# Kernel optimization log

Hardware: AMD Instinct MI355X
Metric: run time of the kernel (lower is better)

The kernel has to match this reference:

```python
import jax, jax.numpy as jnp
import numpy as np

LN_EPS = 1e-5

def _layernorm(x, g, b):
    mu = jnp.mean(x, axis=-1, keepdims=True)
    var = jnp.var(x, axis=-1, keepdims=True)
    return (x - mu) * jax.lax.rsqrt(var + LN_EPS) * g + b

def setup_inputs() -> dict:
    key = jax.random.key(0)
    ks = jax.random.split(key, 8)
    B, T, V, H = 32, 128, 204, 128
    s = 0.02
    x = jax.random.normal(ks[0], (B, T, V, 1), dtype=jnp.float32)
    return {
        "x": x,
        # batched per-variable GRN params
        "fc1_w": jax.random.normal(ks[1], (V, H), dtype=jnp.float32) * s,
        "fc1_b": jnp.zeros((V, H), jnp.float32),
        "fc2_w": jax.random.normal(ks[2], (V, H, H), dtype=jnp.float32) * s,
        "fc2_b": jnp.zeros((V, H), jnp.float32),
        "glu_w": jax.random.normal(ks[3], (V, 2 * H, H), dtype=jnp.float32) * s,
        "glu_b": jnp.zeros((V, 2 * H), jnp.float32),
        "skip_w": jax.random.normal(ks[4], (V, H), dtype=jnp.float32) * s,
        "skip_b": jnp.zeros((V, H), jnp.float32),
        "ln_g": jnp.ones((H,), jnp.float32),
        "ln_b": jnp.zeros((H,), jnp.float32),
        # weight GRN params (input_dim=V, hidden=H, output_dim=V; identity skip)
        "wfc1_w": jax.random.normal(ks[5], (V, H), dtype=jnp.float32) * s,
        "wfc1_b": jnp.zeros((H,), jnp.float32),
        "wfc2_w": jax.random.normal(ks[6], (H, H), dtype=jnp.float32) * s,
        "wfc2_b": jnp.zeros((H,), jnp.float32),
        "wglu_w": jax.random.normal(ks[7], (H, 2 * V), dtype=jnp.float32) * s,
        "wglu_b": jnp.zeros((2 * V,), jnp.float32),
        "wln_g": jnp.ones((V,), jnp.float32),
        "wln_b": jnp.zeros((V,), jnp.float32),
    }

def reference(x, fc1_w, fc1_b, fc2_w, fc2_b, glu_w, glu_b, skip_w, skip_b, ln_g, ln_b,
              wfc1_w, wfc1_b, wfc2_w, wfc2_b, wglu_w, wglu_b, wln_g, wln_b):
    B, T, V, D = x.shape
    H = fc1_w.shape[1]
    xs = x.reshape(B * T, V)  # (N, V) since D == 1

    # --- batched per-variable GRN (eval mode: dropout is identity) ---
    h = jax.nn.elu(xs[..., None] * fc1_w + fc1_b)              # (N, V, H)
    h = jnp.einsum('nvh,vhk->nvk', h, fc2_w) + fc2_b           # bmm over V
    glu = jnp.einsum('nvh,vgh->nvg', h, glu_w) + glu_b         # (N, V, 2H)
    fc_out, gate = glu[..., :H], glu[..., H:]
    h = fc_out * jax.nn.sigmoid(gate)
    skip = xs[..., None] * skip_w + skip_b                     # (N, V, H)
    var_out = _layernorm(skip + h, ln_g, ln_b)                 # (N, V, H)

    # --- weight GRN (input_dim = output_dim = V -> identity skip) ---
    a = jax.nn.elu(xs @ wfc1_w + wfc1_b)                       # (N, H)
    a = a @ wfc2_w + wfc2_b
    g = a @ wglu_w + wglu_b                                    # (N, 2V)
    hg = g[:, :V] * jax.nn.sigmoid(g[:, V:])
    wts = jax.nn.softmax(_layernorm(xs + hg, wln_g, wln_b), axis=-1)  # (N, V)

    out = jnp.einsum('nvh,nv->nh', var_out, wts)               # (N, H)
    return out.reshape(B, T, H), wts.reshape(B, T, V)
```

## Files before the change

### kernel.cpp

```cpp
#include <hip/hip_runtime.h>
#include <hip/hip_bf16.h>

#define NROWS 4096
#define NV    204
#define NH    128
#define NG    256

#define SLOT_B     16384
#define SMS_OFF    (3 * SLOT_B)
#define SMS_BYTES  3584
#define LN_OFF     (SMS_OFF + 2 * SMS_BYTES)
#define LDS_BYTES  (LN_OFF + 1024)

typedef __bf16 bf16x8 __attribute__((ext_vector_type(8)));
typedef float  f32x4  __attribute__((ext_vector_type(4)));

__device__ __forceinline__ float elu_f(float x)  { return x > 0.f ? x : __expf(x) - 1.f; }
__device__ __forceinline__ float sigm_f(float x) { return 1.f / (1.f + __expf(-x)); }

__device__ __forceinline__ void stage16(const void* g, void* l) {
    __builtin_amdgcn_global_load_lds((const __attribute__((address_space(1))) void*)g,
                                     (__attribute__((address_space(3))) void*)l, 16, 0, 0);
}

__device__ __forceinline__ void stage_half(const void* src, char* dst, int w, int l) {
    const char* sb = (const char*)src;
    #pragma unroll
    for (int s = 0; s < 4; ++s)
        stage16(sb + (w * 4 + s) * 1024 + l * 16, dst + (w * 4 + s) * 1024);
}

__device__ __forceinline__ void stage_smalls(const float* src, char* dst, int w, int l) {
    if (w < 3)       stage16((const char*)src + w * 1024 + l * 16, dst + w * 1024);
    else if (l < 32) stage16((const char*)src + 3072 + l * 16,     dst + 3072);
}

#define PSYNC(N) do { \
    asm volatile("s_waitcnt vmcnt(" N ")" ::: "memory"); \
    __builtin_amdgcn_s_barrier(); \
    asm volatile("" ::: "memory"); \
} while (0)

#define NB_FC2 NV
#define NB_GLU (NV * 16)
#define NB_SM  NV
#define NB_WTS (NROWS / 8)

__global__ __launch_bounds__(256) void k_setup(
    const float* __restrict__ fc2_w, __bf16* __restrict__ fc2t,
    const float* __restrict__ glu_w, __bf16* __restrict__ glu16,
    const float* __restrict__ fc1_w, const float* __restrict__ fc1_b,
    const float* __restrict__ fc2_b, const float* __restrict__ glu_b,
    const float* __restrict__ skip_w, const float* __restrict__ skip_b,
    float* __restrict__ smalls,
    const float* __restrict__ xs,
    const float* __restrict__ wfc1_w, const float* __restrict__ wfc1_b,
    const float* __restrict__ wfc2_w, const float* __restrict__ wfc2_b,
    const float* __restrict__ wglu_w, const float* __restrict__ wglu_b,
    const float* __restrict__ wln_g,  const float* __restrict__ wln_b,
    float* __restrict__ wts)
{
    __shared__ float tile[64 * 129];
    __shared__ float sx[8][NV];
    __shared__ float sa[8][NH];
    __shared__ float sg[8][2 * NV];

    const int b = blockIdx.x;
    const int t = threadIdx.x;

    if (b < NB_FC2) {
        const int v = b;
        const float* s = fc2_w + (size_t)v * (NH * NH);
        __bf16*      d = fc2t + (size_t)v * (NH * NH);
        for (int h = 0; h < 2; ++h) {
            __syncthreads();
            for (int i = t; i < 64 * 32; i += 256) {
                const int k = i >> 5, n4 = (i & 31) * 4;
                const float4 f = *(const float4*)(s + (h * 64 + k) * 128 + n4);
                tile[k * 129 + n4 + 0] = f.x;
                tile[k * 129 + n4 + 1] = f.y;
                tile[k * 129 + n4 + 2] = f.z;
                tile[k * 129 + n4 + 3] = f.w;
            }
            __syncthreads();
            for (int i = t; i < 128 * 8; i += 256) {
                const int n = i >> 3, kc = (i & 7) * 8;
                bf16x8 o;
                #pragma unroll
                for (int q = 0; q < 8; ++q) o[q] = (__bf16)tile[(kc + q) * 129 + n];
                const int ch  = h * 8 + (i & 7);
                const int chs = ch ^ (n & 15);
                *(bf16x8*)(d + n * 128 + chs * 8) = o;
            }
        }
        return;
    }

    if (b < NB_FC2 + NB_GLU) {
        const int idx = (b - NB_FC2) * 256 + t;
        const int ch = idx & 15;
        const int g  = (idx >> 4) & 255;
        const int v  = idx >> 12;
        const float* sp = glu_w + (((size_t)v * NG + g) * NH + ch * 8);
        const float4 f0 = *(const float4*)(sp);
        const float4 f1 = *(const float4*)(sp + 4);
        bf16x8 o;
        o[0] = (__bf16)f0.x; o[1] = (__bf16)f0.y; o[2] = (__bf16)f0.z; o[3] = (__bf16)f0.w;
        o[4] = (__bf16)f1.x; o[5] = (__bf16)f1.y; o[6] = (__bf16)f1.z; o[7] = (__bf16)f1.w;
        const int dch = ch ^ (g & 15);
        *(bf16x8*)(glu16 + (((size_t)v * NG + g) * NH) + dch * 8) = o;
        return;
    }

    if (b < NB_FC2 + NB_GLU + NB_SM) {
        const int v = b - (NB_FC2 + NB_GLU);
        float* dst = smalls + (size_t)v * 1024;
        for (int idx = t; idx < 896; idx += 256) {
            float val;
            if      (idx < 128)  val = fc1_w[v * NH + idx];
            else if (idx < 256)  val = fc1_b[v * NH + idx - 128];
            else if (idx < 384)  val = fc2_b[v * NH + idx - 256];
            else if (idx < 640)  val = glu_b[v * NG + idx - 384];
            else if (idx < 768)  val = skip_w[v * NH + idx - 640];
            else                 val = skip_b[v * NH + idx - 768];
            dst[idx] = val;
        }
        return;
    }

    const int r0 = (b - NB_FC2 - NB_GLU - NB_SM) * 8;
    const int tr = t >> 5;
    const int tc = t & 31;

    for (int i = t; i < 8 * NV; i += 256) {
        const int r = i / NV, c = i - r * NV;
        sx[r][c] = xs[(size_t)(r0 + r) * NV + c];
    }
    __syncthreads();

    float acc1[4];
    #pragma unroll
    for (int j = 0; j < 4; ++j) acc1[j] = wfc1_b[tc + 32 * j];
    for (int v = 0; v < NV; ++v) {
        const float xv = sx[tr][v];
        #pragma unroll
        for (int j = 0; j < 4; ++j)
            acc1[j] = fmaf(xv, wfc1_w[v * NH + tc + 32 * j], acc1[j]);
    }
    #pragma unroll
    for (int j = 0; j < 4; ++j) sa[tr][tc + 32 * j] = elu_f(acc1[j]);
    __syncthreads();

    float acc2[4];
    #pragma unroll
    for (int j = 0; j < 4; ++j) acc2[j] = wfc2_b[tc + 32 * j];
    for (int h = 0; h < NH; ++h) {
        const float av = sa[tr][h];
        #pragma unroll
        for (int j = 0; j < 4; ++j)
            acc2[j] = fmaf(av, wfc2_w[h * NH + tc + 32 * j], acc2[j]);
    }
    __syncthreads();
    #pragma unroll
    for (int j = 0; j < 4; ++j) sa[tr][tc + 32 * j] = acc2[j];
    __syncthreads();

    float accg[13];
    #pragma unroll
    for (int gi = 0; gi < 12; ++gi) accg[gi] = wglu_b[tc + 32 * gi];
    accg[12] = (tc < 24) ? wglu_b[tc + 384] : 0.f;
    for (int h = 0; h < NH; ++h) {
        const float av = sa[tr][h];
        #pragma unroll
        for (int gi = 0; gi < 12; ++gi)
            accg[gi] = fmaf(av, wglu_w[h * (2 * NV) + tc + 32 * gi], accg[gi]);
        if (tc < 24) accg[12] = fmaf(av, wglu_w[h * (2 * NV) + tc + 384], accg[12]);
    }
    __syncthreads();
    #pragma unroll
    for (int gi = 0; gi < 12; ++gi) sg[tr][tc + 32 * gi] = accg[gi];
    if (tc < 24) sg[tr][tc + 384] = accg[12];
    __syncthreads();

    float tv[7];
    float s1 = 0.f, s2 = 0.f;
    #pragma unroll
    for (int ii = 0; ii < 7; ++ii) {
        const int c = tc + 32 * ii;
        float val = 0.f;
        if (c < NV) {
            const float hg = sg[tr][c] * sigm_f(sg[tr][c + NV]);
            val = sx[tr][c] + hg;
            s1 += val; s2 = fmaf(val, val, s2);
        }
        tv[ii] = val;
    }
    #pragma unroll
    for (int m = 1; m <= 16; m <<= 1) { s1 += __shfl_xor(s1, m); s2 += __shfl_xor(s2, m); }
    const float mu  = s1 * (1.f / 204.f);
    const float var = s2 * (1.f / 204.f) - mu * mu;
    const float rs  = rsqrtf(fmaxf(var, 0.f) + 1e-5f);

    float mx = -1e30f;
    #pragma unroll
    for (int ii = 0; ii < 7; ++ii) {
        const int c = tc + 32 * ii;
        if (c < NV) {
            const float y = fmaf((tv[ii] - mu) * rs, wln_g[c], wln_b[c]);
            tv[ii] = y;
            mx = fmaxf(mx, y);
        }
    }
    #pragma unroll
    for (int m = 1; m <= 16; m <<= 1) mx = fmaxf(mx, __shfl_xor(mx, m));
    float se = 0.f;
    #pragma unroll
    for (int ii = 0; ii < 7; ++ii) {
        const int c = tc + 32 * ii;
        if (c < NV) {
            const float e = __expf(tv[ii] - mx);
            tv[ii] = e;
            se += e;
        }
    }
    #pragma unroll
    for (int m = 1; m <= 16; m <<= 1) se += __shfl_xor(se, m);
    const float inv = 1.f / se;
    #pragma unroll
    for (int ii = 0; ii < 7; ++ii) {
        const int c = tc + 32 * ii;
        if (c < NV) wts[(size_t)(r0 + tr) * NV + c] = tv[ii] * inv;
    }
}

__global__ __launch_bounds__(256, 2) void k_main(
    const float*  __restrict__ xs,
    const __bf16* __restrict__ fc2t,
    const __bf16* __restrict__ glu16,
    const float*  __restrict__ smalls,
    const float*  __restrict__ ln_g,
    const float*  __restrict__ ln_b,
    const float*  __restrict__ wts,
    float*        __restrict__ out)
{
    __shared__ __align__(16) char lds[LDS_BYTES];

    const int tid = threadIdx.x;
    const int w   = tid >> 6;
    const int l   = tid & 63;
    const int l15 = l & 15;
    const int lg  = l >> 4;

    const int vg = blockIdx.x & 7;
    const int m0 = (blockIdx.x >> 3) * 64 + w * 16;
    const int nv = (NV - 1 - vg) / 8 + 1;
    const size_t rowoff = (size_t)(m0 + l15) * NV;

    char* const slot0 = lds;
    char* const slot1 = lds + SLOT_B;
    char* const slot2 = lds + 2 * SLOT_B;

    const f32x4 zero4 = {0.f, 0.f, 0.f, 0.f};
    f32x4 acc_out[8];
    #pragma unroll
    for (int j = 0; j < 8; ++j) acc_out[j] = zero4;

    const int  sh0 = l15 + ((lg & 1) << 5);
    const int  sh1 = sh0 + 16;
    const bool rlo = (lg < 2);

    const float* lnS = (const float*)(lds + LN_OFF);

    float xv, wv, xn, wn;
    {
        if (w == 0) {
            const char* p = (l < 32) ? ((const char*)ln_g + l * 16)
                                     : ((const char*)ln_b + (l - 32) * 16);
            stage16(p, lds + LN_OFF);
        }
        stage_half(fc2t + (size_t)vg * (NH * NH), slot0, w, l);
        stage_smalls(smalls + (size_t)vg * 1024, lds + SMS_OFF, w, l);
        stage_half(fc2t + (size_t)vg * (NH * NH) + 64 * NH, slot1, w, l);
        xv = xs[rowoff + vg];
        wv = wts[rowoff + vg];
    }

    for (int i = 0; i < nv; ++i) {
        const int v  = vg + 8 * i;
        const int vn = (i + 1 < nv) ? v + 8 : v;
        const float* sm = (const float*)(lds + SMS_OFF + (i & 1) * SMS_BYTES);
        const __bf16* gluv = glu16 + (size_t)v * (NG * NH);

        PSYNC("6");
        stage_half(gluv, slot2, w, l);

        bf16x8 a1[4];
        #pragma unroll
        for (int kb = 0; kb < 4; ++kb) {
            const int k0 = kb * 32 + lg * 8;
            const float4 w0 = *(const float4*)(sm + k0);
            const float4 w1 = *(const float4*)(sm + k0 + 4);
            const float4 b0 = *(const float4*)(sm + 128 + k0);
            const float4 b1 = *(const float4*)(sm + 128 + k0 + 4);
            bf16x8 af;
            af[0] = (__bf16)elu_f(fmaf(xv, w0.x, b0.x));
            af[1] = (__bf16)elu_f(fmaf(xv, w0.y, b0.y));
            af[2] = (__bf16)elu_f(fmaf(xv, w0.z, b0.z));
            af[3] = (__bf16)elu_f(fmaf(xv, w0.w, b0.w));
            af[4] = (__bf16)elu_f(fmaf(xv, w1.x, b1.x));
            af[5] = (__bf16)elu_f(fmaf(xv, w1.y, b1.y));
            af[6] = (__bf16)elu_f(fmaf(xv, w1.z, b1.z));
            af[7] = (__bf16)elu_f(fmaf(xv, w1.w, b1.w));
            a1[kb] = af;
        }

        f32x4 h2f[8];
        __builtin_amdgcn_s_setprio(1);
        #pragma unroll
        for (int j = 0; j < 4; ++j) {
            f32x4 acc = *(const f32x4*)(sm + 256 + j * 16 + lg * 4);
            const char* rp = slot0 + (j * 16 + l15) * 256;
            #pragma unroll
            for (int kb = 0; kb < 4; ++kb) {
                const bf16x8 wf = *(const bf16x8*)(rp + (((kb * 4 + lg) ^ l15) << 4));
                acc = __builtin_amdgcn_mfma_f32_16x16x32_bf16(wf, a1[kb], acc, 0, 0, 0);
            }
            h2f[j] = acc;
        }
        __builtin_amdgcn_s_setprio(0);

        PSYNC("6");
        stage_half(gluv + 64 * NH, slot0, w, l);

        __builtin_amdgcn_s_setprio(1);
        #pragma unroll
        for (int j = 4; j < 8; ++j) {
            f32x4 acc = *(const f32x4*)(sm + 256 + j * 16 + lg * 4);
            const char* rp = slot1 + ((j - 4) * 16 + l15) * 256;
            #pragma unroll
            for (int kb = 0; kb < 4; ++kb) {
                const bf16x8 wf = *(const bf16x8*)(rp + (((kb * 4 + lg) ^ l15) << 4));
                acc = __builtin_amdgcn_mfma_f32_16x16x32_bf16(wf, a1[kb], acc, 0, 0, 0);
            }
            h2f[j] = acc;
        }
        __builtin_amdgcn_s_setprio(0);

        bf16x8 b2[4];
        #pragma unroll
        for (int kb2 = 0; kb2 < 4; ++kb2) {
            union U { __bf16 h[4]; int i2[2]; };
            U P, Q;
            P.h[0] = (__bf16)h2f[2 * kb2 + 0][0]; P.h[1] = (__bf16)h2f[2 * kb2 + 0][1];
            P.h[2] = (__bf16)h2f[2 * kb2 + 0][2]; P.h[3] = (__bf16)h2f[2 * kb2 + 0][3];
            Q.h[0] = (__bf16)h2f[2 * kb2 + 1][0]; Q.h[1] = (__bf16)h2f[2 * kb2 + 1][1];
            Q.h[2] = (__bf16)h2f[2 * kb2 + 1][2]; Q.h[3] = (__bf16)h2f[2 * kb2 + 1][3];
            const int px0 = __shfl(P.i2[0], sh0), qx0 = __shfl(Q.i2[0], sh0);
            const int py0 = __shfl(P.i2[1], sh0), qy0 = __shfl(Q.i2[1], sh0);
            const int px1 = __shfl(P.i2[0], sh1), qx1 = __shfl(Q.i2[0], sh1);
            const int py1 = __shfl(P.i2[1], sh1), qy1 = __shfl(Q.i2[1], sh1);
            union V { int ii[4]; bf16x8 vv; } R;
            R.ii[0] = rlo ? px0 : qx0;
            R.ii[1] = rlo ? py0 : qy0;
            R.ii[2] = rlo ? px1 : qx1;
            R.ii[3] = rlo ? py1 : qy1;
            b2[kb2] = R.vv;
        }

        PSYNC("4");
        stage_half(gluv + 128 * NH, slot1, w, l);

        f32x4 fco[8];
        __builtin_amdgcn_s_setprio(1);
        #pragma unroll
        for (int j = 0; j < 4; ++j) {
            f32x4 acc = *(const f32x4*)(sm + 384 + j * 16 + lg * 4);
            const char* rp = slot2 + (j * 16 + l15) * 256;
            #pragma unroll
            for (int kb = 0; kb < 4; ++kb) {
                const bf16x8 wf = *(const bf16x8*)(rp + (((kb * 4 + lg) ^ l15) << 4));
                acc = __builtin_amdgcn_mfma_f32_16x16x32_bf16(wf, b2[kb], acc, 0, 0, 0);
            }
            fco[j] = acc;
        }
        __builtin_amdgcn_s_setprio(0);

        PSYNC("4");
        stage_half(gluv + 192 * NH, slot2, w, l);

        __builtin_amdgcn_s_setprio(1);
        #pragma unroll
        for (int j = 4; j < 8; ++j) {
            f32x4 acc = *(const f32x4*)(sm + 384 + j * 16 + lg * 4);
            const char* rp = slot0 + ((j - 4) * 16 + l15) * 256;
            #pragma unroll
            for (int kb = 0; kb < 4; ++kb) {
                const bf16x8 wf = *(const bf16x8*)(rp + (((kb * 4 + lg) ^ l15) << 4));
                acc = __builtin_amdgcn_mfma_f32_16x16x32_bf16(wf, b2[kb], acc, 0, 0, 0);
            }
            fco[j] = acc;
        }
        __builtin_amdgcn_s_setprio(0);

        PSYNC("4");
        stage_half(fc2t + (size_t)vn * (NH * NH), slot0, w, l);

        f32x4 sv[8];
        __builtin_amdgcn_s_setprio(1);
        #pragma unroll
        for (int j = 0; j < 4; ++j) {
            f32x4 acc = *(const f32x4*)(sm + 512 + j * 16 + lg * 4);
            const char* rp = slot1 + (j * 16 + l15) * 256;
            #pragma unroll
            for (int kb = 0; kb < 4; ++kb) {
                const bf16x8 wg = *(const bf16x8*)(rp + (((kb * 4 + lg) ^ l15) << 4));
                acc = __builtin_amdgcn_mfma_f32_16x16x32_bf16(wg, b2[kb], acc, 0, 0, 0);
            }
            __builtin_amdgcn_s_setprio(0);
            const float4 sw4 = *(const float4*)(sm + 640 + j * 16 + lg * 4);
            const float4 sb4 = *(const float4*)(sm + 768 + j * 16 + lg * 4);
            f32x4 s;
            s[0] = fmaf(xv, sw4.x, sb4.x) + fco[j][0] * sigm_f(acc[0]);
            s[1] = fmaf(xv, sw4.y, sb4.y) + fco[j][1] * sigm_f(acc[1]);
            s[2] = fmaf(xv, sw4.z, sb4.z) + fco[j][2] * sigm_f(acc[2]);
            s[3] = fmaf(xv, sw4.w, sb4.w) + fco[j][3] * sigm_f(acc[3]);
            sv[j] = s;
            __builtin_amdgcn_s_setprio(1);
        }
        __builtin_amdgcn_s_setprio(0);

        PSYNC("4");
        stage_smalls(smalls + (size_t)vn * 1024,
                     lds + SMS_OFF + ((i + 1) & 1) * SMS_BYTES, w, l);
        stage_half(fc2t + (size_t)vn * (NH * NH) + 64 * NH, slot1, w, l);
        xn = xs[rowoff + vn];
        wn = wts[rowoff + vn];

        __builtin_amdgcn_s_setprio(1);
        #pragma unroll
        for (int j = 4; j < 8; ++j) {
            f32x4 acc = *(const f32x4*)(sm + 512 + j * 16 + lg * 4);
            const char* rp = slot2 + ((j - 4) * 16 + l15) * 256;
            #pragma unroll
            for (int kb = 0; kb < 4; ++kb) {
                const bf16x8 wg = *(const bf16x8*)(rp + (((kb * 4 + lg) ^ l15) << 4));
                acc = __builtin_amdgcn_mfma_f32_16x16x32_bf16(wg, b2[kb], acc, 0, 0, 0);
            }
            __builtin_amdgcn_s_setprio(0);
            const float4 sw4 = *(const float4*)(sm + 640 + j * 16 + lg * 4);
            const float4 sb4 = *(const float4*)(sm + 768 + j * 16 + lg * 4);
            f32x4 s;
            s[0] = fmaf(xv, sw4.x, sb4.x) + fco[j][0] * sigm_f(acc[0]);
            s[1] = fmaf(xv, sw4.y, sb4.y) + fco[j][1] * sigm_f(acc[1]);
            s[2] = fmaf(xv, sw4.z, sb4.z) + fco[j][2] * sigm_f(acc[2]);
            s[3] = fmaf(xv, sw4.w, sb4.w) + fco[j][3] * sigm_f(acc[3]);
            sv[j] = s;
            __builtin_amdgcn_s_setprio(1);
        }
        __builtin_amdgcn_s_setprio(0);

        float t1 = 0.f, t2 = 0.f;
        #pragma unroll
        for (int j = 0; j < 8; ++j) {
            #pragma unroll
            for (int r = 0; r < 4; ++r) { t1 += sv[j][r]; t2 = fmaf(sv[j][r], sv[j][r], t2); }
        }
        t1 += __shfl_xor(t1, 16); t2 += __shfl_xor(t2, 16);
        t1 += __shfl_xor(t1, 32); t2 += __shfl_xor(t2, 32);
        const float mu  = t1 * (1.f / 128.f);
        const float var = t2 * (1.f / 128.f) - mu * mu;
        const float rsv = rsqrtf(fmaxf(var, 0.f) + 1e-5f);

        #pragma unroll
        for (int j = 0; j < 8; ++j) {
            const float4 lg4 = *(const float4*)(lnS + j * 16 + lg * 4);
            const float4 lb4 = *(const float4*)(lnS + 128 + j * 16 + lg * 4);
            const float y0 = fmaf((sv[j][0] - mu) * rsv, lg4.x, lb4.x);
            const float y1 = fmaf((sv[j][1] - mu) * rsv, lg4.y, lb4.y);
            const float y2 = fmaf((sv[j][2] - mu) * rsv, lg4.z, lb4.z);
            const float y3 = fmaf((sv[j][3] - mu) * rsv, lg4.w, lb4.w);
            acc_out[j][0] = fmaf(wv, y0, acc_out[j][0]);
            acc_out[j][1] = fmaf(wv, y1, acc_out[j][1]);
            acc_out[j][2] = fmaf(wv, y2, acc_out[j][2]);
            acc_out[j][3] = fmaf(wv, y3, acc_out[j][3]);
        }

        xv = xn; wv = wn;
    }

    asm volatile("s_waitcnt vmcnt(0)" ::: "memory");

    #pragma unroll
    for (int j = 0; j < 8; ++j) {
        #pragma unroll
        for (int r = 0; r < 4; ++r)
            atomicAdd(&out[(size_t)(m0 + l15) * NH + j * 16 + lg * 4 + r], acc_out[j][r]);
    }
}

extern "C" void kernel_launch(void* const* d_in, const int* in_sizes, int n_in,
                              void* d_out, int out_size, void* d_ws, size_t ws_size,
                              hipStream_t stream) {
    (void)in_sizes; (void)n_in; (void)out_size; (void)ws_size;

    const float* xs     = (const float*)d_in[0];
    const float* fc1_w  = (const float*)d_in[1];
    const float* fc1_b  = (const float*)d_in[2];
    const float* fc2_w  = (const float*)d_in[3];
    const float* fc2_b  = (const float*)d_in[4];
    const float* glu_w  = (const float*)d_in[5];
    const float* glu_b  = (const float*)d_in[6];
    const float* skip_w = (const float*)d_in[7];
    const float* skip_b = (const float*)d_in[8];
    const float* ln_g   = (const float*)d_in[9];
    const float* ln_b   = (const float*)d_in[10];
    const float* wfc1_w = (const float*)d_in[11];
    const float* wfc1_b = (const float*)d_in[12];
    const float* wfc2_w = (const float*)d_in[13];
    const float* wfc2_b = (const float*)d_in[14];
    const float* wglu_w = (const float*)d_in[15];
    const float* wglu_b = (const float*)d_in[16];
    const float* wln_g  = (const float*)d_in[17];
    const float* wln_b  = (const float*)d_in[18];

    float* out = (float*)d_out;
    float* wts = out + (size_t)NROWS * NH;

    __bf16* fc2t   = (__bf16*)d_ws;
    __bf16* glu16  = fc2t + (size_t)NV * NH * NH;
    float*  smalls = (float*)(glu16 + (size_t)NV * NG * NH);

    hipMemsetAsync(d_out, 0, (size_t)NROWS * NH * sizeof(float), stream);

    k_setup<<<NB_FC2 + NB_GLU + NB_SM + NB_WTS, 256, 0, stream>>>(
        fc2_w, fc2t, glu_w, glu16,
        fc1_w, fc1_b, fc2_b, glu_b, skip_w, skip_b, smalls,
        xs, wfc1_w, wfc1_b, wfc2_w, wfc2_b, wglu_w, wglu_b, wln_g, wln_b, wts);

    k_main<<<(NROWS / 64) * 8, 256, 0, stream>>>(xs, fc2t, glu16, smalls,
                                                 ln_g, ln_b, wts, out);
}
```

Baseline: 331.6 us.

## Switch LDS weight staging from three half-slots to ping-pong full-tile pairs

Replaces the rotating three-slot, half-tile staging pipeline with two 32KB slot pairs used ping-pong, so each 128x128 weight matrix is staged whole and a full 8-tile MFMA phase runs per barrier. Barriers per variable drop from six partial-vmcnt waits to three vmcnt(0) waits. The aim is to cut synchronisation overhead, at the cost of more LDS (64KB of slots, which may reduce occupancy) and a coarser prefetch that waits for all outstanding loads at each barrier.

```diff
diff --git a/kernel.cpp b/kernel.cpp
--- a/kernel.cpp
+++ b/kernel.cpp
@@ -7,7 +7,8 @@
 #define NG    256
 
 #define SLOT_B     16384
-#define SMS_OFF    (3 * SLOT_B)
+#define PAIR_B     (2 * SLOT_B)
+#define SMS_OFF    (2 * PAIR_B)
 #define SMS_BYTES  3584
 #define LN_OFF     (SMS_OFF + 2 * SMS_BYTES)
 #define LDS_BYTES  (LN_OFF + 1024)
@@ -35,8 +36,8 @@
     else if (l < 32) stage16((const char*)src + 3072 + l * 16,     dst + 3072);
 }
 
-#define PSYNC(N) do { \
-    asm volatile("s_waitcnt vmcnt(" N ")" ::: "memory"); \
+#define PSYNC0() do { \
+    asm volatile("s_waitcnt vmcnt(0)" ::: "memory"); \
     __builtin_amdgcn_s_barrier(); \
     asm volatile("" ::: "memory"); \
 } while (0)
@@ -256,10 +257,6 @@
     const int nv = (NV - 1 - vg) / 8 + 1;
     const size_t rowoff = (size_t)(m0 + l15) * NV;
 
-    char* const slot0 = lds;
-    char* const slot1 = lds + SLOT_B;
-    char* const slot2 = lds + 2 * SLOT_B;
-
     const f32x4 zero4 = {0.f, 0.f, 0.f, 0.f};
     f32x4 acc_out[8];
     #pragma unroll
@@ -278,9 +275,9 @@
                                      : ((const char*)ln_b + (l - 32) * 16);
             stage16(p, lds + LN_OFF);
         }
-        stage_half(fc2t + (size_t)vg * (NH * NH), slot0, w, l);
+        stage_half(fc2t + (size_t)vg * (NH * NH), lds, w, l);
+        stage_half(fc2t + (size_t)vg * (NH * NH) + 64 * NH, lds + SLOT_B, w, l);
         stage_smalls(smalls + (size_t)vg * 1024, lds + SMS_OFF, w, l);
-        stage_half(fc2t + (size_t)vg * (NH * NH) + 64 * NH, slot1, w, l);
         xv = xs[rowoff + vg];
         wv = wts[rowoff + vg];
     }
@@ -291,8 +288,12 @@
         const float* sm = (const float*)(lds + SMS_OFF + (i & 1) * SMS_BYTES);
         const __bf16* gluv = glu16 + (size_t)v * (NG * NH);
 
-        PSYNC("6");
-        stage_half(gluv, slot2, w, l);
+        char* const pF = lds + ((i & 1) ? PAIR_B : 0);
+        char* const pC = lds + ((i & 1) ? 0 : PAIR_B);
+
+        PSYNC0();
+        stage_half(gluv,           pC,          w, l);
+        stage_half(gluv + 64 * NH, pC + SLOT_B, w, l);
 
         bf16x8 a1[4];
         #pragma unroll
@@ -317,26 +318,9 @@
         f32x4 h2f[8];
         __builtin_amdgcn_s_setprio(1);
         #pragma unroll
-        for (int j = 0; j < 4; ++j) {
+        for (int j = 0; j < 8; ++j) {
             f32x4 acc = *(const f32x4*)(sm + 256 + j * 16 + lg * 4);
-            const char* rp = slot0 + (j * 16 + l15) * 256;
-            #pragma unroll
-            for (int kb = 0; kb < 4; ++kb) {
-                const bf16x8 wf = *(const bf16x8*)(rp + (((kb * 4 + lg) ^ l15) << 4));
-                acc = __builtin_amdgcn_mfma_f32_16x16x32_bf16(wf, a1[kb], acc, 0, 0, 0);
-            }
-            h2f[j] = acc;
-        }
-        __builtin_amdgcn_s_setprio(0);
-
-        PSYNC("6");
-        stage_half(gluv + 64 * NH, slot0, w, l);
-
-        __builtin_amdgcn_s_setprio(1);
-        #pragma unroll
-        for (int j = 4; j < 8; ++j) {
-            f32x4 acc = *(const f32x4*)(sm + 256 + j * 16 + lg * 4);
-            const char* rp = slot1 + ((j - 4) * 16 + l15) * 256;
+            const char* rp = (j < 4 ? pF : pF + SLOT_B) + ((j & 3) * 16 + l15) * 256;
             #pragma unroll
             for (int kb = 0; kb < 4; ++kb) {
                 const bf16x8 wf = *(const bf16x8*)(rp + (((kb * 4 + lg) ^ l15) << 4));
@@ -367,15 +351,16 @@
             b2[kb2] = R.vv;
         }
 
-        PSYNC("4");
-        stage_half(gluv + 128 * NH, slot1, w, l);
+        PSYNC0();
+        stage_half(gluv + 128 * NH, pF,          w, l);
+        stage_half(gluv + 192 * NH, pF + SLOT_B, w, l);
 
         f32x4 fco[8];
         __builtin_amdgcn_s_setprio(1);
         #pragma unroll
-        for (int j = 0; j < 4; ++j) {
+        for (int j = 0; j < 8; ++j) {
             f32x4 acc = *(const f32x4*)(sm + 384 + j * 16 + lg * 4);
-            const char* rp = slot2 + (j * 16 + l15) * 256;
+            const char* rp = (j < 4 ? pC : pC + SLOT_B) + ((j & 3) * 16 + l15) * 256;
             #pragma unroll
             for (int kb = 0; kb < 4; ++kb) {
                 const bf16x8 wf = *(const bf16x8*)(rp + (((kb * 4 + lg) ^ l15) << 4));
@@ -385,62 +370,20 @@
         }
         __builtin_amdgcn_s_setprio(0);
 
-        PSYNC("4");
-        stage_half(gluv + 192 * NH, slot2, w, l);
-
-        __builtin_amdgcn_s_setprio(1);
-        #pragma unroll
-        for (int j = 4; j < 8; ++j) {
-            f32x4 acc = *(const f32x4*)(sm + 384 + j * 16 + lg * 4);
-            const char* rp = slot0 + ((j - 4) * 16 + l15) * 256;
-            #pragma unroll
-            for (int kb = 0; kb < 4; ++kb) {
-                const bf16x8 wf = *(const bf16x8*)(rp + (((kb * 4 + lg) ^ l15) << 4));
-                acc = __builtin_amdgcn_mfma_f32_16x16x32_bf16(wf, b2[kb], acc, 0, 0, 0);
-            }
-            fco[j] = acc;
-        }
-        __builtin_amdgcn_s_setprio(0);
-
-        PSYNC("4");
-        stage_half(fc2t + (size_t)vn * (NH * NH), slot0, w, l);
+        PSYNC0();
+        stage_half(fc2t + (size_t)vn * (NH * NH),           pC,          w, l);
+        stage_half(fc2t + (size_t)vn * (NH * NH) + 64 * NH, pC + SLOT_B, w, l);
+        stage_smalls(smalls + (size_t)vn * 1024,
+                     lds + SMS_OFF + ((i + 1) & 1) * SMS_BYTES, w, l);
+        xn = xs[rowoff + vn];
+        wn = wts[rowoff + vn];
 
         f32x4 sv[8];
         __builtin_amdgcn_s_setprio(1);
         #pragma unroll
-        for (int j = 0; j < 4; ++j) {
+        for (int j = 0; j < 8; ++j) {
             f32x4 acc = *(const f32x4*)(sm + 512 + j * 16 + lg * 4);
-            const char* rp = slot1 + (j * 16 + l15) * 256;
-            #pragma unroll
-            for (int kb = 0; kb < 4; ++kb) {
-                const bf16x8 wg = *(const bf16x8*)(rp + (((kb * 4 + lg) ^ l15) << 4));
-                acc = __builtin_amdgcn_mfma_f32_16x16x32_bf16(wg, b2[kb], acc, 0, 0, 0);
-            }
-            __builtin_amdgcn_s_setprio(0);
-            const float4 sw4 = *(const float4*)(sm + 640 + j * 16 + lg * 4);
-            const float4 sb4 = *(const float4*)(sm + 768 + j * 16 + lg * 4);
-            f32x4 s;
-            s[0] = fmaf(xv, sw4.x, sb4.x) + fco[j][0] * sigm_f(acc[0]);
-            s[1] = fmaf(xv, sw4.y, sb4.y) + fco[j][1] * sigm_f(acc[1]);
-            s[2] = fmaf(xv, sw4.z, sb4.z) + fco[j][2] * sigm_f(acc[2]);
-            s[3] = fmaf(xv, sw4.w, sb4.w) + fco[j][3] * sigm_f(acc[3]);
-            sv[j] = s;
-            __builtin_amdgcn_s_setprio(1);
-        }
-        __builtin_amdgcn_s_setprio(0);
-
-        PSYNC("4");
-        stage_smalls(smalls + (size_t)vn * 1024,
-                     lds + SMS_OFF + ((i + 1) & 1) * SMS_BYTES, w, l);
-        stage_half(fc2t + (size_t)vn * (NH * NH) + 64 * NH, slot1, w, l);
-        xn = xs[rowoff + vn];
-        wn = wts[rowoff + vn];
-
-        __builtin_amdgcn_s_setprio(1);
-        #pragma unroll
-        for (int j = 4; j < 8; ++j) {
-            f32x4 acc = *(const f32x4*)(sm + 512 + j * 16 + lg * 4);
-            const char* rp = slot2 + ((j - 4) * 16 + l15) * 256;
+            const char* rp = (j < 4 ? pF : pF + SLOT_B) + ((j & 3) * 16 + l15) * 256;
             #pragma unroll
             for (int kb = 0; kb < 4; ++kb) {
                 const bf16x8 wg = *(const bf16x8*)(rp + (((kb * 4 + lg) ^ l15) << 4));
```

Result: no change. 334.5 us (+0.9%).
